# Kernel tuning notes

Measured on AMD Instinct MI355X. Metric: run time of the kernel, lower is better.

Reference implementation:

```python
import jax, jax.numpy as jnp
import numpy as np

DIM = 1024
NUM_HEADS = 16
HEAD_DIM = DIM // NUM_HEADS
SCALE = HEAD_DIM ** -0.5


def setup_inputs() -> dict:
    key = jax.random.key(0)
    k1, k2, k3, k4 = jax.random.split(key, 4)
    x = jax.random.normal(k1, (4, 2048, DIM), dtype=jnp.float32)
    # nn.Linear weights: out = x @ W.T + b ; store as [out, in] like torch
    w_qkv = jax.random.normal(k2, (3 * DIM, DIM), dtype=jnp.float32) * (DIM ** -0.5)
    w_proj = jax.random.normal(k3, (DIM, DIM), dtype=jnp.float32) * (DIM ** -0.5)
    b_proj = jax.random.normal(k4, (DIM,), dtype=jnp.float32) * 0.01
    return {"x": x, "w_qkv": w_qkv, "w_proj": w_proj, "b_proj": b_proj}


def reference(x, w_qkv, w_proj, b_proj):
    B, N, C = x.shape
    H, D = NUM_HEADS, HEAD_DIM
    qkv = jnp.einsum('bnc,oc->bno', x, w_qkv)            # [B,N,3C]
    qkv = qkv.reshape(B, N, 3, H, D).transpose(2, 0, 3, 1, 4)  # [3,B,H,N,D]
    q, k, v = qkv[0] * SCALE, qkv[1], qkv[2]
    attn = jax.nn.softmax(jnp.einsum('bhnd,bhmd->bhnm', q, k), axis=-1)
    out = jnp.einsum('bhnm,bhmd->bhnd', attn, v)          # [B,H,N,D]
    out = out.transpose(0, 2, 1, 3).reshape(B, N, C)
    return jnp.einsum('bnc,oc->bno', out, w_proj) + b_proj
```

## Files before the change

kernel.cpp:

```cpp
#include <hip/hip_runtime.h>
#include <cstdint>

#define DIM   1024
#define NH    16
#define HD    64
#define SEQ   2048
#define BATCH 4
#define QK_EXP2_SCALE 0.18033688011112042f

typedef _Float16 half8  __attribute__((ext_vector_type(8)));
typedef __fp16   fp16x2 __attribute__((ext_vector_type(2)));
typedef float    f32x4  __attribute__((ext_vector_type(4)));

#define GLOBAL_AS __attribute__((address_space(1)))
#define LDS_AS    __attribute__((address_space(3)))

__device__ __forceinline__ ushort f2h(float f) {
  union { _Float16 h; ushort u; } c; c.h = (_Float16)f; return c.u;
}
__device__ __forceinline__ void async_cp16(const ushort* g, ushort* l) {
  __builtin_amdgcn_global_load_lds((const GLOBAL_AS uint32_t*)g,
                                   (LDS_AS uint32_t*)l, 16, 0, 0);
}

__global__ __launch_bounds__(256) void cvt3_f32_to_f16(
    const float4* __restrict__ x, const float4* __restrict__ wq,
    const float4* __restrict__ wp, ushort4* __restrict__ xo,
    ushort4* __restrict__ wqo, ushort4* __restrict__ wpo) {
  int i = blockIdx.x * 256 + threadIdx.x;
  const float4* src; ushort4* dst; int j;
  if (i < 2097152)      { src = x;  dst = xo;  j = i; }
  else if (i < 2883584) { src = wq; dst = wqo; j = i - 2097152; }
  else                  { src = wp; dst = wpo; j = i - 2883584; }
  float4 v = src[j];
  dst[j] = make_ushort4(f2h(v.x), f2h(v.y), f2h(v.z), f2h(v.w));
}

__global__ __launch_bounds__(256, 2) void gemm_bt256(
    const ushort* __restrict__ A, const ushort* __restrict__ Bt,
    ushort* __restrict__ Ch, int M, int N, int K) {
  __shared__ ushort As[128 * 64];
  __shared__ ushort Bs[256 * 64];
  const int t    = threadIdx.x;
  const int w    = t >> 6;
  const int lane = t & 63;
  const int quad = lane >> 4;
  const int l16  = lane & 15;
  const int wm   = w >> 1, wn = w & 1;

  const int num_n = N >> 8;
  const int SUPER = 8;
  const int bid   = blockIdx.x;
  const int strip = bid / (SUPER * num_n);
  const int rem   = bid % (SUPER * num_n);
  const int m0 = (strip * SUPER + (rem % SUPER)) * 128;
  const int n0 = (rem / SUPER) * 256;

  f32x4 acc[4][8];
  #pragma unroll
  for (int it = 0; it < 4; ++it)
    #pragma unroll
    for (int jt = 0; jt < 8; ++jt) acc[it][jt] = (f32x4){0, 0, 0, 0};

  const int srow = lane >> 3;
  const int scol = (lane & 7) * 8;

  for (int k0 = 0; k0 < K; k0 += 64) {
    __syncthreads();
    #pragma unroll
    for (int p = 0; p < 4; ++p) {
      const int rbase = w * 32 + p * 8;
      async_cp16(&A[(size_t)(m0 + rbase + srow) * K + k0 + scol], &As[rbase * 64]);
    }
    #pragma unroll
    for (int p = 0; p < 8; ++p) {
      const int rbase = w * 64 + p * 8;
      async_cp16(&Bt[(size_t)(n0 + rbase + srow) * K + k0 + scol], &Bs[rbase * 64]);
    }
    __syncthreads();
    #pragma unroll
    for (int kk = 0; kk < 2; ++kk) {
      half8 a[4];
      #pragma unroll
      for (int it = 0; it < 4; ++it)
        a[it] = *(const half8*)&As[(wm * 64 + it * 16 + l16) * 64 + kk * 32 + quad * 8];
      #pragma unroll
      for (int jt = 0; jt < 8; ++jt) {
        half8 b = *(const half8*)&Bs[(wn * 128 + jt * 16 + l16) * 64 + kk * 32 + quad * 8];
        #pragma unroll
        for (int it = 0; it < 4; ++it)
          acc[it][jt] = __builtin_amdgcn_mfma_f32_16x16x32_f16(a[it], b, acc[it][jt], 0, 0, 0);
      }
    }
  }

  #pragma unroll
  for (int it = 0; it < 4; ++it)
    #pragma unroll
    for (int jt = 0; jt < 8; ++jt)
      #pragma unroll
      for (int i = 0; i < 4; ++i) {
        int row = m0 + wm * 64 + it * 16 + quad * 4 + i;
        int col = n0 + wn * 128 + jt * 16 + l16;
        Ch[(size_t)row * N + col] = f2h(acc[it][jt][i]);
      }
}

__global__ __launch_bounds__(256) void gemm_bt128(
    const ushort* __restrict__ A, const ushort* __restrict__ Bt,
    float* __restrict__ Cf, const float* __restrict__ bias,
    int M, int N, int K) {
  __shared__ ushort As[128 * 64];
  __shared__ ushort Bs[128 * 64];
  const int t    = threadIdx.x;
  const int w    = t >> 6;
  const int lane = t & 63;
  const int quad = lane >> 4;
  const int l16  = lane & 15;
  const int wm   = w >> 1, wn = w & 1;

  const int num_n = N >> 7;
  const int SUPER = 8;
  const int bid   = blockIdx.x;
  const int strip = bid / (SUPER * num_n);
  const int rem   = bid % (SUPER * num_n);
  const int m0 = (strip * SUPER + (rem % SUPER)) * 128;
  const int n0 = (rem / SUPER) * 128;

  f32x4 acc[4][4];
  #pragma unroll
  for (int it = 0; it < 4; ++it)
    #pragma unroll
    for (int jt = 0; jt < 4; ++jt) acc[it][jt] = (f32x4){0, 0, 0, 0};

  const int srow = lane >> 3;
  const int scol = (lane & 7) * 8;

  for (int k0 = 0; k0 < K; k0 += 64) {
    __syncthreads();
    #pragma unroll
    for (int p = 0; p < 4; ++p) {
      const int rbase = w * 32 + p * 8;
      async_cp16(&A[(size_t)(m0 + rbase + srow) * K + k0 + scol], &As[rbase * 64]);
      async_cp16(&Bt[(size_t)(n0 + rbase + srow) * K + k0 + scol], &Bs[rbase * 64]);
    }
    __syncthreads();
    #pragma unroll
    for (int kk = 0; kk < 2; ++kk) {
      half8 a[4], b[4];
      #pragma unroll
      for (int it = 0; it < 4; ++it)
        a[it] = *(const half8*)&As[(wm * 64 + it * 16 + l16) * 64 + kk * 32 + quad * 8];
      #pragma unroll
      for (int jt = 0; jt < 4; ++jt)
        b[jt] = *(const half8*)&Bs[(wn * 64 + jt * 16 + l16) * 64 + kk * 32 + quad * 8];
      #pragma unroll
      for (int it = 0; it < 4; ++it)
        #pragma unroll
        for (int jt = 0; jt < 4; ++jt)
          acc[it][jt] = __builtin_amdgcn_mfma_f32_16x16x32_f16(a[it], b[jt], acc[it][jt], 0, 0, 0);
    }
  }

  #pragma unroll
  for (int it = 0; it < 4; ++it)
    #pragma unroll
    for (int jt = 0; jt < 4; ++jt)
      #pragma unroll
      for (int i = 0; i < 4; ++i) {
        int row = m0 + wm * 64 + it * 16 + quad * 4 + i;
        int col = n0 + wn * 64 + jt * 16 + l16;
        Cf[(size_t)row * N + col] = acc[it][jt][i] + bias[col];
      }
}

__global__ __launch_bounds__(256, 2) void attn_mfma(
    const ushort* __restrict__ qkv, ushort* __restrict__ attn_out) {
  constexpr int LDT = 68;
  __shared__ ushort Qs[256 * LDT];
  __shared__ ushort Ks[2][64 * LDT];
  __shared__ ushort Vt[2][64 * LDT];

  const int t    = threadIdx.x;
  const int w    = t >> 6;
  const int lane = t & 63;
  const int quad = lane >> 4;
  const int l16  = lane & 15;
  const int q0 = blockIdx.x * 256;
  const int h  = blockIdx.y;
  const int b  = blockIdx.z;

  const int srow = t >> 2;
  const int sseg = t & 3;
  const int vp   = t & 31;
  const int vs   = t >> 5;
  const int vpos = ((vp >> 4) << 5) + (((vp >> 1) & 3) << 3)
                 + (((vp >> 3) & 1) << 2) + ((vp & 1) << 1);

  #pragma unroll
  for (int pass = 0; pass < 2; ++pass) {
    const int qrow = pass * 128 + (t >> 1), qseg = t & 1;
    const ushort* qp = qkv + (size_t)(b * SEQ + q0 + qrow) * (3 * DIM)
                       + h * HD + qseg * 32;
    #pragma unroll
    for (int e = 0; e < 4; ++e)
      *(int4*)&Qs[qrow * LDT + qseg * 32 + e * 8] = *(const int4*)(qp + e * 8);
  }

  f32x4 ot[4][4];
  float lacc[4] = {0.0f, 0.0f, 0.0f, 0.0f};
  #pragma unroll
  for (int qt = 0; qt < 4; ++qt)
    #pragma unroll
    for (int nt = 0; nt < 4; ++nt) ot[qt][nt] = (f32x4){0, 0, 0, 0};

  for (int c = 0; c < SEQ / 64; ++c) {
    const int k0 = c * 64;
    const int buf = c & 1;
    {
      const ushort* kp = qkv + (size_t)(b * SEQ + k0 + srow) * (3 * DIM)
                         + DIM + h * HD + sseg * 16;
      *(int4*)&Ks[buf][srow * LDT + sseg * 16 + 0] = *(const int4*)(kp + 0);
      *(int4*)&Ks[buf][srow * LDT + sseg * 16 + 8] = *(const int4*)(kp + 8);
    }
    {
      const ushort* vb = qkv + (size_t)(b * SEQ + k0) * (3 * DIM)
                         + 2 * DIM + h * HD + vs * 8;
      union { int4 v; ushort u[8]; } r0, r1;
      r0.v = *(const int4*)(vb + (size_t)(2 * vp)     * (3 * DIM));
      r1.v = *(const int4*)(vb + (size_t)(2 * vp + 1) * (3 * DIM));
      #pragma unroll
      for (int j = 0; j < 8; ++j) {
        uint pk = (uint)r0.u[j] | ((uint)r1.u[j] << 16);
        *(uint*)&Vt[buf][(vs * 8 + j) * LDT + vpos] = pk;
      }
    }
    __syncthreads();

    f32x4 st[4][4];
    #pragma unroll
    for (int qt = 0; qt < 4; ++qt)
      #pragma unroll
      for (int kt = 0; kt < 4; ++kt) st[qt][kt] = (f32x4){0, 0, 0, 0};
    #pragma unroll
    for (int kk = 0; kk < 2; ++kk) {
      half8 kfr[4], qfr[4];
      #pragma unroll
      for (int kt = 0; kt < 4; ++kt)
        kfr[kt] = *(const half8*)&Ks[buf][(kt * 16 + l16) * LDT + kk * 32 + quad * 8];
      #pragma unroll
      for (int qt = 0; qt < 4; ++qt)
        qfr[qt] = *(const half8*)&Qs[(w * 64 + qt * 16 + l16) * LDT + kk * 32 + quad * 8];
      #pragma unroll
      for (int qt = 0; qt < 4; ++qt)
        #pragma unroll
        for (int kt = 0; kt < 4; ++kt)
          st[qt][kt] = __builtin_amdgcn_mfma_f32_16x16x32_f16(kfr[kt], qfr[qt], st[qt][kt], 0, 0, 0);
    }

    union { half8 h; uint u[4]; } pf[4][2];
    #pragma unroll
    for (int qt = 0; qt < 4; ++qt) {
      float p[4][4];
      #pragma unroll
      for (int kt = 0; kt < 4; ++kt)
        #pragma unroll
        for (int i = 0; i < 4; ++i) {
          p[kt][i] = __builtin_amdgcn_exp2f(st[qt][kt][i] * QK_EXP2_SCALE);
          lacc[qt] += p[kt][i];
        }
      #pragma unroll
      for (int kc = 0; kc < 2; ++kc) {
        union { fp16x2 h; uint u; } c01, c23, c45, c67;
        c01.h = __builtin_amdgcn_cvt_pkrtz(p[2 * kc][0], p[2 * kc][1]);
        c23.h = __builtin_amdgcn_cvt_pkrtz(p[2 * kc][2], p[2 * kc][3]);
        c45.h = __builtin_amdgcn_cvt_pkrtz(p[2 * kc + 1][0], p[2 * kc + 1][1]);
        c67.h = __builtin_amdgcn_cvt_pkrtz(p[2 * kc + 1][2], p[2 * kc + 1][3]);
        pf[qt][kc].u[0] = c01.u; pf[qt][kc].u[1] = c23.u;
        pf[qt][kc].u[2] = c45.u; pf[qt][kc].u[3] = c67.u;
      }
    }

    #pragma unroll
    for (int kc = 0; kc < 2; ++kc) {
      half8 vfr[4];
      #pragma unroll
      for (int nt = 0; nt < 4; ++nt)
        vfr[nt] = *(const half8*)&Vt[buf][(nt * 16 + l16) * LDT + kc * 32 + quad * 8];
      #pragma unroll
      for (int qt = 0; qt < 4; ++qt)
        #pragma unroll
        for (int nt = 0; nt < 4; ++nt)
          ot[qt][nt] = __builtin_amdgcn_mfma_f32_16x16x32_f16(vfr[nt], pf[qt][kc].h, ot[qt][nt], 0, 0, 0);
    }
  }

  __syncthreads();
  #pragma unroll
  for (int qt = 0; qt < 4; ++qt) {
    float lsum = lacc[qt];
    lsum += __shfl_xor(lsum, 16);
    lsum += __shfl_xor(lsum, 32);
    float inv = 1.0f / lsum;
    #pragma unroll
    for (int nt = 0; nt < 4; ++nt)
      #pragma unroll
      for (int i = 0; i < 4; ++i)
        Qs[(w * 64 + qt * 16 + l16) * LDT + nt * 16 + quad * 4 + i] =
            f2h(ot[qt][nt][i] * inv);
  }
  __syncthreads();
  #pragma unroll
  for (int pass = 0; pass < 2; ++pass) {
    const int orow = pass * 128 + (t >> 1), oseg = t & 1;
    size_t gbase = (size_t)(b * SEQ + q0 + orow) * DIM + h * HD + oseg * 32;
    #pragma unroll
    for (int e = 0; e < 4; ++e)
      *(int4*)&attn_out[gbase + e * 8] = *(const int4*)&Qs[orow * LDT + oseg * 32 + e * 8];
  }
}

extern "C" void kernel_launch(void* const* d_in, const int* in_sizes, int n_in,
                              void* d_out, int out_size, void* d_ws, size_t ws_size,
                              hipStream_t stream) {
  const float* x      = (const float*)d_in[0];
  const float* w_qkv  = (const float*)d_in[1];
  const float* w_proj = (const float*)d_in[2];
  const float* b_proj = (const float*)d_in[3];

  char* ws = (char*)d_ws;
  ushort* x_h   = (ushort*)(ws + 0);
  ushort* wq_h  = (ushort*)(ws + 16777216);
  ushort* wp_h  = (ushort*)(ws + 23068672);
  ushort* qkv_h = (ushort*)(ws + 25165824);
  ushort* at_h  = (ushort*)(ws + 75497472);

  cvt3_f32_to_f16<<<12288, 256, 0, stream>>>(
      (const float4*)x, (const float4*)w_qkv, (const float4*)w_proj,
      (ushort4*)x_h, (ushort4*)wq_h, (ushort4*)wp_h);

  gemm_bt256<<<64 * 12, 256, 0, stream>>>(x_h, wq_h, qkv_h, 8192, 3072, 1024);
  attn_mfma<<<dim3(8, 16, 4), 256, 0, stream>>>(qkv_h, at_h);
  gemm_bt128<<<64 * 8, 256, 0, stream>>>(at_h, wp_h, (float*)d_out,
                                         b_proj, 8192, 1024, 1024);
}
```

Before: 277.4 us.

## Prefetch next K/V tile into registers, fold QK scale into QKV GEMM epilogue

The attention loop now loads the next K/V tile from global memory into registers before computing on the current tile, and writes it into the other LDS buffer after the PV MFMAs. This hides global load latency behind compute, at the cost of extra registers that may lower occupancy. The QK exp2 scale is folded into the QKV GEMM epilogue for the Q columns, which removes a multiply per score. s_setprio is raised around the MFMA blocks.

```diff
diff --git a/kernel.cpp b/kernel.cpp
--- a/kernel.cpp
+++ b/kernel.cpp
@@ -97,13 +97,16 @@
   #pragma unroll
   for (int it = 0; it < 4; ++it)
     #pragma unroll
-    for (int jt = 0; jt < 8; ++jt)
+    for (int jt = 0; jt < 8; ++jt) {
+      const int colbase = n0 + wn * 128 + jt * 16;
+      const float qs = (colbase < DIM) ? QK_EXP2_SCALE : 1.0f;
       #pragma unroll
       for (int i = 0; i < 4; ++i) {
         int row = m0 + wm * 64 + it * 16 + quad * 4 + i;
         int col = n0 + wn * 128 + jt * 16 + l16;
-        Ch[(size_t)row * N + col] = f2h(acc[it][jt][i]);
-      }
+        Ch[(size_t)row * N + col] = f2h(acc[it][jt][i] * qs);
+      }
+    }
 }
 
 __global__ __launch_bounds__(256) void gemm_bt128(
@@ -214,34 +217,47 @@
     #pragma unroll
     for (int nt = 0; nt < 4; ++nt) ot[qt][nt] = (f32x4){0, 0, 0, 0};
 
+  const ushort* kbase = qkv + (size_t)(b * SEQ + srow) * (3 * DIM)
+                        + DIM + h * HD + sseg * 16;
+  const ushort* vbase = qkv + (size_t)(b * SEQ + 2 * vp) * (3 * DIM)
+                        + 2 * DIM + h * HD + vs * 8;
+  const size_t tstep = (size_t)64 * (3 * DIM);
+
+  int4 kr0 = *(const int4*)(kbase + 0);
+  int4 kr1 = *(const int4*)(kbase + 8);
+  int4 vr0 = *(const int4*)(vbase);
+  int4 vr1 = *(const int4*)(vbase + 3 * DIM);
+  {
+    *(int4*)&Ks[0][srow * LDT + sseg * 16 + 0] = kr0;
+    *(int4*)&Ks[0][srow * LDT + sseg * 16 + 8] = kr1;
+    union { int4 v; ushort u[8]; } r0, r1;
+    r0.v = vr0; r1.v = vr1;
+    #pragma unroll
+    for (int j = 0; j < 8; ++j) {
+      uint pk = (uint)r0.u[j] | ((uint)r1.u[j] << 16);
+      *(uint*)&Vt[0][(vs * 8 + j) * LDT + vpos] = pk;
+    }
+  }
+
   for (int c = 0; c < SEQ / 64; ++c) {
-    const int k0 = c * 64;
     const int buf = c & 1;
-    {
-      const ushort* kp = qkv + (size_t)(b * SEQ + k0 + srow) * (3 * DIM)
-                         + DIM + h * HD + sseg * 16;
-      *(int4*)&Ks[buf][srow * LDT + sseg * 16 + 0] = *(const int4*)(kp + 0);
-      *(int4*)&Ks[buf][srow * LDT + sseg * 16 + 8] = *(const int4*)(kp + 8);
-    }
-    {
-      const ushort* vb = qkv + (size_t)(b * SEQ + k0) * (3 * DIM)
-                         + 2 * DIM + h * HD + vs * 8;
-      union { int4 v; ushort u[8]; } r0, r1;
-      r0.v = *(const int4*)(vb + (size_t)(2 * vp)     * (3 * DIM));
-      r1.v = *(const int4*)(vb + (size_t)(2 * vp + 1) * (3 * DIM));
-      #pragma unroll
-      for (int j = 0; j < 8; ++j) {
-        uint pk = (uint)r0.u[j] | ((uint)r1.u[j] << 16);
-        *(uint*)&Vt[buf][(vs * 8 + j) * LDT + vpos] = pk;
-      }
-    }
-    __syncthreads();
+    __syncthreads();
+
+    if (c + 1 < SEQ / 64) {
+      const ushort* kp = kbase + (size_t)(c + 1) * tstep;
+      const ushort* vv = vbase + (size_t)(c + 1) * tstep;
+      kr0 = *(const int4*)(kp + 0);
+      kr1 = *(const int4*)(kp + 8);
+      vr0 = *(const int4*)(vv);
+      vr1 = *(const int4*)(vv + 3 * DIM);
+    }
 
     f32x4 st[4][4];
     #pragma unroll
     for (int qt = 0; qt < 4; ++qt)
       #pragma unroll
       for (int kt = 0; kt < 4; ++kt) st[qt][kt] = (f32x4){0, 0, 0, 0};
+    __builtin_amdgcn_s_setprio(1);
     #pragma unroll
     for (int kk = 0; kk < 2; ++kk) {
       half8 kfr[4], qfr[4];
@@ -257,6 +273,7 @@
         for (int kt = 0; kt < 4; ++kt)
           st[qt][kt] = __builtin_amdgcn_mfma_f32_16x16x32_f16(kfr[kt], qfr[qt], st[qt][kt], 0, 0, 0);
     }
+    __builtin_amdgcn_s_setprio(0);
 
     union { half8 h; uint u[4]; } pf[4][2];
     #pragma unroll
@@ -266,7 +283,7 @@
       for (int kt = 0; kt < 4; ++kt)
         #pragma unroll
         for (int i = 0; i < 4; ++i) {
-          p[kt][i] = __builtin_amdgcn_exp2f(st[qt][kt][i] * QK_EXP2_SCALE);
+          p[kt][i] = __builtin_amdgcn_exp2f(st[qt][kt][i]);
           lacc[qt] += p[kt][i];
         }
       #pragma unroll
@@ -281,6 +298,7 @@
       }
     }
 
+    __builtin_amdgcn_s_setprio(1);
     #pragma unroll
     for (int kc = 0; kc < 2; ++kc) {
       half8 vfr[4];
@@ -292,6 +310,20 @@
         #pragma unroll
         for (int nt = 0; nt < 4; ++nt)
           ot[qt][nt] = __builtin_amdgcn_mfma_f32_16x16x32_f16(vfr[nt], pf[qt][kc].h, ot[qt][nt], 0, 0, 0);
+    }
+    __builtin_amdgcn_s_setprio(0);
+
+    if (c + 1 < SEQ / 64) {
+      const int nb = buf ^ 1;
+      *(int4*)&Ks[nb][srow * LDT + sseg * 16 + 0] = kr0;
+      *(int4*)&Ks[nb][srow * LDT + sseg * 16 + 8] = kr1;
+      union { int4 v; ushort u[8]; } r0, r1;
+      r0.v = vr0; r1.v = vr1;
+      #pragma unroll
+      for (int j = 0; j < 8; ++j) {
+        uint pk = (uint)r0.u[j] | ((uint)r1.u[j] << 16);
+        *(uint*)&Vt[nb][(vs * 8 + j) * LDT + vpos] = pk;
+      }
     }
   }
 
```

Measured after the change: 271.1 us. -2.3%, faster.
